# Kernel tuning notes

Hardware: AMD Instinct MI355X
Metric: run time of the kernel (lower is better)

## Reference

```python
import jax, jax.numpy as jnp
import numpy as np

EMB_DIM = 512
NUM_HEADS = 8
HEAD_DIM = EMB_DIM // NUM_HEADS


def setup_inputs() -> dict:
    key = jax.random.key(0)
    ks = jax.random.split(key, 8)
    B, S, D = 2, 192, EMB_DIM
    return {
        "q": jax.random.normal(ks[0], (B, S, D), dtype=jnp.float32),
        "k": jax.random.normal(ks[1], (B, S, D), dtype=jnp.float32),
        "l": jax.random.normal(ks[2], (B, S, D), dtype=jnp.float32),
        "v": jax.random.normal(ks[3], (B, S, D), dtype=jnp.float32),
        "Wq": jax.random.normal(ks[4], (D, D), dtype=jnp.float32) * (1.0 / np.sqrt(D)),
        "Wk": jax.random.normal(ks[5], (D, D), dtype=jnp.float32) * (1.0 / np.sqrt(D)),
        "Wv": jax.random.normal(ks[6], (D, D), dtype=jnp.float32) * (1.0 / np.sqrt(D)),
        "Wout": jax.random.normal(ks[7], (D, D), dtype=jnp.float32) * (1.0 / np.sqrt(D)),
    }


def _heads(x, W):
    # torch nn.Linear: x @ W.T ; then split heads -> (B, H, S, hd)
    B, S, D = x.shape
    y = x @ W.T
    return y.reshape(B, S, NUM_HEADS, HEAD_DIM).transpose(0, 2, 1, 3)


def reference(q, k, l, v, Wq, Wk, Wv, Wout):
    B, QS, D = q.shape
    KS, LS = k.shape[1], l.shape[1]
    qh = _heads(q, Wq)
    kh = _heads(k, Wk)
    lh = _heads(l, Wk)  # NOTE: original module projects l with self.key (faithful)
    vh = _heads(v, Wv)
    # rank-3 attention scores: (B, H, QS, KS, LS)
    scores = jnp.einsum('bhqe,bhke,bhle->bhqkl', qh, kh, lh) / jnp.sqrt(
        jnp.asarray(HEAD_DIM, dtype=q.dtype))
    # softmax jointly over (KS, LS)
    attn = jax.nn.softmax(scores.reshape(B, NUM_HEADS, QS, KS * LS), axis=-1)
    attn = attn.reshape(B, NUM_HEADS, QS, KS, LS)
    # vv[b,h,l,k,d] = v[b,h,k,d]; contract over k and l -> (B, QS, H, hd)
    attended = jnp.einsum('bhqkl,bhkd->bqhd', attn, vh)
    concatenated = attended.reshape(B, QS, EMB_DIM)
    return concatenated @ Wout.T
```

## Files before the change

### kernel.cpp

```cpp
#include <hip/hip_runtime.h>
#include <math.h>

#define BB 2
#define SS 192
#define DD 512
#define HH 8
#define HD 64
#define QCB 6
#define NQC (SS / QCB)
#define PROJ_N (BB*HH*SS*HD)
#define SCL (0.125f * 1.44269504088896f)

typedef __attribute__((ext_vector_type(4))) float f32x4;
typedef _Float16 f16x8 __attribute__((ext_vector_type(8)));

__device__ __forceinline__ f16x8 cvt8_f16_rne(const float* g) {
    f16x8 r;
#pragma unroll
    for (int i = 0; i < 8; ++i) r[i] = (_Float16)g[i];
    return r;
}

__global__ __launch_bounds__(256) void proj4_kernel(
    const float* __restrict__ xq, const float* __restrict__ xk,
    const float* __restrict__ xl, const float* __restrict__ xv,
    const float* __restrict__ Wq, const float* __restrict__ Wk,
    const float* __restrict__ Wv, float* __restrict__ ws,
    float* __restrict__ out) {
    const int p = blockIdx.z;
    const float* x = (p == 0) ? xq : (p == 1) ? xk : (p == 2) ? xl : xv;
    const float* W = (p == 0) ? Wq : (p == 3) ? Wv : Wk;
    float* y = ws + p * PROJ_N;

    __shared__ short Ahs[2][8 * 64 * 8];
    __shared__ short Bhs[2][8 * 64 * 8];

    const int t = threadIdx.x;

    {
        const int bid = (blockIdx.z * gridDim.y + blockIdx.y) * gridDim.x + blockIdx.x;
        for (int i = bid * 256 + t; i < BB * SS * DD; i += 192 * 256) out[i] = 0.f;
    }

    const int lane = t & 63, w = t >> 6;
    const int wr = w >> 1, wc = w & 1;
    const int c16 = lane & 15, q4 = lane >> 4;
    const int m0 = blockIdx.x * 64, n0 = blockIdx.y * 64;
    const int r = t >> 2, cc = t & 3;

    f32x4 acc[2][2];
#pragma unroll
    for (int a = 0; a < 2; ++a)
#pragma unroll
        for (int b = 0; b < 2; ++b) acc[a][b] = (f32x4){0.f, 0.f, 0.f, 0.f};

#define STAGE(kk, bf)                                                               \
    {                                                                               \
        _Pragma("unroll") for (int h2 = 0; h2 < 2; ++h2) {                          \
            const int ec = cc * 2 + h2;                                             \
            float a8[8], w8[8];                                                     \
            *(f32x4*)&a8[0] = *(const f32x4*)&x[(m0 + r) * 512 + (kk) + ec * 8];    \
            *(f32x4*)&a8[4] = *(const f32x4*)&x[(m0 + r) * 512 + (kk) + ec * 8 + 4];\
            *(f32x4*)&w8[0] = *(const f32x4*)&W[(n0 + r) * 512 + (kk) + ec * 8];    \
            *(f32x4*)&w8[4] = *(const f32x4*)&W[(n0 + r) * 512 + (kk) + ec * 8 + 4];\
            *(f16x8*)&Ahs[bf][(ec * 64 + r) * 8] = cvt8_f16_rne(a8);                \
            *(f16x8*)&Bhs[bf][(ec * 64 + r) * 8] = cvt8_f16_rne(w8);                \
        }                                                                           \
    }

    STAGE(0, 0)
    for (int s = 0; s < 8; ++s) {
        __syncthreads();
        if (s + 1 < 8) STAGE((s + 1) * 64, (s + 1) & 1)
        const int b = s & 1;
        f16x8 aH[2][2], bH[2][2];
#pragma unroll
        for (int mt = 0; mt < 2; ++mt) {
            const int row = wr * 32 + mt * 16 + c16;
            aH[mt][0] = *(const f16x8*)&Ahs[b][(q4 * 64 + row) * 8];
            aH[mt][1] = *(const f16x8*)&Ahs[b][((q4 + 4) * 64 + row) * 8];
        }
#pragma unroll
        for (int nt = 0; nt < 2; ++nt) {
            const int col = wc * 32 + nt * 16 + c16;
            bH[nt][0] = *(const f16x8*)&Bhs[b][(q4 * 64 + col) * 8];
            bH[nt][1] = *(const f16x8*)&Bhs[b][((q4 + 4) * 64 + col) * 8];
        }
#pragma unroll
        for (int mt = 0; mt < 2; ++mt)
#pragma unroll
            for (int nt = 0; nt < 2; ++nt) {
                acc[mt][nt] = __builtin_amdgcn_mfma_f32_16x16x32_f16(aH[mt][0], bH[nt][0], acc[mt][nt], 0, 0, 0);
                acc[mt][nt] = __builtin_amdgcn_mfma_f32_16x16x32_f16(aH[mt][1], bH[nt][1], acc[mt][nt], 0, 0, 0);
            }
    }
#undef STAGE

#pragma unroll
    for (int mt = 0; mt < 2; ++mt)
#pragma unroll
        for (int nt = 0; nt < 2; ++nt)
#pragma unroll
            for (int j = 0; j < 4; ++j) {
                const int n_row = m0 + wr * 32 + mt * 16 + q4 * 4 + j;
                const int col = n0 + wc * 32 + nt * 16 + c16;
                const int b = n_row / SS, s2 = n_row % SS;
                const int h = col >> 6, e = col & 63;
                y[((b * HH + h) * SS + s2) * HD + e] = acc[mt][nt][j];
            }
}

__global__ __launch_bounds__(512, 4) void attn3d_mfma_kernel(
    const float* __restrict__ qh, const float* __restrict__ kh,
    const float* __restrict__ lh, const float* __restrict__ vh,
    const float* __restrict__ Wout, float* __restrict__ out) {
    __shared__ short Kf16[8][193][8];
    __shared__ short Lf16[8][193][8];
    __shared__ short qpk[QCB][8][8];
    __shared__ float partial[2][QCB][196];
    __shared__ float Wt[QCB][192];
    __shared__ float attd[16][72];
    __shared__ float zinv[QCB];

    const int blk = blockIdx.x;
    const int bh = blk >> 5, qc = blk & 31;
    const int t = threadIdx.x;
    const int lane = t & 63, w = t >> 6;
    const int lg = w >> 2, kg = w & 3;
    const int c = lane & 15, eh = lane >> 4;

    if (t < QCB * 64) {
        const int q = t >> 6, e = t & 63;
        const float v = qh[(bh * SS + qc * QCB + q) * HD + e] * SCL;
        qpk[q][e >> 3][e & 7] = __builtin_bit_cast(short, (_Float16)v);
    }
#pragma unroll
    for (int j = 0; j < 3; ++j) {
        const int cid = t + 512 * j;
        const int k = cid >> 3, ec = cid & 7;
        float b8[8];
        const float* kp = &kh[(bh * SS + k) * HD + ec * 8];
        *(f32x4*)&b8[0] = *(const f32x4*)&kp[0];
        *(f32x4*)&b8[4] = *(const f32x4*)&kp[4];
        *(f16x8*)&Kf16[ec][k][0] = cvt8_f16_rne(b8);
        const float* lp = &lh[(bh * SS + k) * HD + ec * 8];
        *(f32x4*)&b8[0] = *(const f32x4*)&lp[0];
        *(f32x4*)&b8[4] = *(const f32x4*)&lp[4];
        *(f16x8*)&Lf16[ec][k][0] = cvt8_f16_rne(b8);
    }
    __syncthreads();

    for (int qpi = 0; qpi < 3; ++qpi) {
        const int qa = (qpi + w) % 3;
        const int qb = qa + 3;
        const f16x8 qaf0 = *(const f16x8*)&qpk[qa][eh][0];
        const f16x8 qaf1 = *(const f16x8*)&qpk[qa][4 + eh][0];
        const f16x8 qbf0 = *(const f16x8*)&qpk[qb][eh][0];
        const f16x8 qbf1 = *(const f16x8*)&qpk[qb][4 + eh][0];
        f16x8 Ba[3][2], Bb[3][2];
#pragma unroll
        for (int kt = 0; kt < 3; ++kt) {
            const int col = kg * 48 + kt * 16 + c;
            const f16x8 Kf0 = *(const f16x8*)&Kf16[eh][col][0];
            const f16x8 Kf1 = *(const f16x8*)&Kf16[4 + eh][col][0];
            Ba[kt][0] = Kf0 * qaf0;
            Ba[kt][1] = Kf1 * qaf1;
            Bb[kt][0] = Kf0 * qbf0;
            Bb[kt][1] = Kf1 * qbf1;
        }
        float ra0 = 0.f, ra1 = 0.f, ra2 = 0.f;
        float rb0 = 0.f, rb1 = 0.f, rb2 = 0.f;
#pragma unroll
        for (int lt = 0; lt < 6; ++lt) {
            const int row = lg * 96 + lt * 16 + c;
            const f16x8 A0 = *(const f16x8*)&Lf16[eh][row][0];
            const f16x8 A1 = *(const f16x8*)&Lf16[4 + eh][row][0];
            f32x4 a0 = (f32x4){0.f, 0.f, 0.f, 0.f};
            f32x4 a1 = (f32x4){0.f, 0.f, 0.f, 0.f};
            f32x4 a2 = (f32x4){0.f, 0.f, 0.f, 0.f};
            f32x4 b0 = (f32x4){0.f, 0.f, 0.f, 0.f};
            f32x4 b1 = (f32x4){0.f, 0.f, 0.f, 0.f};
            f32x4 b2 = (f32x4){0.f, 0.f, 0.f, 0.f};
            a0 = __builtin_amdgcn_mfma_f32_16x16x32_f16(A0, Ba[0][0], a0, 0, 0, 0);
            a1 = __builtin_amdgcn_mfma_f32_16x16x32_f16(A0, Ba[1][0], a1, 0, 0, 0);
            a2 = __builtin_amdgcn_mfma_f32_16x16x32_f16(A0, Ba[2][0], a2, 0, 0, 0);
            b0 = __builtin_amdgcn_mfma_f32_16x16x32_f16(A0, Bb[0][0], b0, 0, 0, 0);
            b1 = __builtin_amdgcn_mfma_f32_16x16x32_f16(A0, Bb[1][0], b1, 0, 0, 0);
            b2 = __builtin_amdgcn_mfma_f32_16x16x32_f16(A0, Bb[2][0], b2, 0, 0, 0);
            a0 = __builtin_amdgcn_mfma_f32_16x16x32_f16(A1, Ba[0][1], a0, 0, 0, 0);
            a1 = __builtin_amdgcn_mfma_f32_16x16x32_f16(A1, Ba[1][1], a1, 0, 0, 0);
            a2 = __builtin_amdgcn_mfma_f32_16x16x32_f16(A1, Ba[2][1], a2, 0, 0, 0);
            b0 = __builtin_amdgcn_mfma_f32_16x16x32_f16(A1, Bb[0][1], b0, 0, 0, 0);
            b1 = __builtin_amdgcn_mfma_f32_16x16x32_f16(A1, Bb[1][1], b1, 0, 0, 0);
            b2 = __builtin_amdgcn_mfma_f32_16x16x32_f16(A1, Bb[2][1], b2, 0, 0, 0);
            ra0 += (__builtin_amdgcn_exp2f(a0[0]) + __builtin_amdgcn_exp2f(a0[1])) +
                   (__builtin_amdgcn_exp2f(a0[2]) + __builtin_amdgcn_exp2f(a0[3]));
            ra1 += (__builtin_amdgcn_exp2f(a1[0]) + __builtin_amdgcn_exp2f(a1[1])) +
                   (__builtin_amdgcn_exp2f(a1[2]) + __builtin_amdgcn_exp2f(a1[3]));
            ra2 += (__builtin_amdgcn_exp2f(a2[0]) + __builtin_amdgcn_exp2f(a2[1])) +
                   (__builtin_amdgcn_exp2f(a2[2]) + __builtin_amdgcn_exp2f(a2[3]));
            rb0 += (__builtin_amdgcn_exp2f(b0[0]) + __builtin_amdgcn_exp2f(b0[1])) +
                   (__builtin_amdgcn_exp2f(b0[2]) + __builtin_amdgcn_exp2f(b0[3]));
            rb1 += (__builtin_amdgcn_exp2f(b1[0]) + __builtin_amdgcn_exp2f(b1[1])) +
                   (__builtin_amdgcn_exp2f(b1[2]) + __builtin_amdgcn_exp2f(b1[3]));
            rb2 += (__builtin_amdgcn_exp2f(b2[0]) + __builtin_amdgcn_exp2f(b2[1])) +
                   (__builtin_amdgcn_exp2f(b2[2]) + __builtin_amdgcn_exp2f(b2[3]));
        }
        ra0 += __shfl_xor(ra0, 16, 64);
        ra1 += __shfl_xor(ra1, 16, 64);
        ra2 += __shfl_xor(ra2, 16, 64);
        rb0 += __shfl_xor(rb0, 16, 64);
        rb1 += __shfl_xor(rb1, 16, 64);
        rb2 += __shfl_xor(rb2, 16, 64);
        ra0 += __shfl_xor(ra0, 32, 64);
        ra1 += __shfl_xor(ra1, 32, 64);
        ra2 += __shfl_xor(ra2, 32, 64);
        rb0 += __shfl_xor(rb0, 32, 64);
        rb1 += __shfl_xor(rb1, 32, 64);
        rb2 += __shfl_xor(rb2, 32, 64);
        if (eh == 0) {
            partial[lg][qa][kg * 48 + 0 * 16 + c] = ra0;
            partial[lg][qa][kg * 48 + 1 * 16 + c] = ra1;
            partial[lg][qa][kg * 48 + 2 * 16 + c] = ra2;
            partial[lg][qb][kg * 48 + 0 * 16 + c] = rb0;
            partial[lg][qb][kg * 48 + 1 * 16 + c] = rb1;
            partial[lg][qb][kg * 48 + 2 * 16 + c] = rb2;
        }
    }
    __syncthreads();

    for (int id = t; id < QCB * 192; id += 512) {
        const int q = id / 192, k = id - q * 192;
        Wt[q][k] = partial[0][q][k] + partial[1][q][k];
    }
    for (int id = t; id < 16 * 72; id += 512) ((float*)attd)[id] = 0.f;
    __syncthreads();

    if (w < QCB) {
        const int q = w;
        float z = Wt[q][lane] + Wt[q][lane + 64] + Wt[q][lane + 128];
#pragma unroll
        for (int off = 32; off >= 1; off >>= 1) z += __shfl_xor(z, off, 64);
        if (lane == 0) zinv[q] = 1.f / z;
    }
    __syncthreads();

    if (t < QCB * 64) {
        const int q = t >> 6, d = t & 63;
        const float* vp = vh + bh * SS * HD + d;
        float sum = 0.f;
        for (int k0 = 0; k0 < SS; k0 += 8) {
            float v8[8];
#pragma unroll
            for (int j = 0; j < 8; ++j) v8[j] = vp[(k0 + j) * HD];
#pragma unroll
            for (int j = 0; j < 8; ++j) sum = fmaf(Wt[q][k0 + j], v8[j], sum);
        }
        attd[q][d] = sum * zinv[q];
    }
    __syncthreads();

    const int b = bh >> 3, h = bh & 7;
    f16x8 Ae0, Ae1;
    {
        float a8[8];
        *(f32x4*)&a8[0] = *(const f32x4*)&attd[c][eh * 8];
        *(f32x4*)&a8[4] = *(const f32x4*)&attd[c][eh * 8 + 4];
        Ae0 = cvt8_f16_rne(a8);
        *(f32x4*)&a8[0] = *(const f32x4*)&attd[c][32 + eh * 8];
        *(f32x4*)&a8[4] = *(const f32x4*)&attd[c][32 + eh * 8 + 4];
        Ae1 = cvt8_f16_rne(a8);
    }
#pragma unroll
    for (int jt = 0; jt < 4; ++jt) {
        const int j = (w * 4 + jt) * 16 + c;
        const float* wp = &Wout[j * DD + h * HD];
        float b8[8];
        *(f32x4*)&b8[0] = *(const f32x4*)&wp[eh * 8];
        *(f32x4*)&b8[4] = *(const f32x4*)&wp[eh * 8 + 4];
        const f16x8 B0 = cvt8_f16_rne(b8);
        *(f32x4*)&b8[0] = *(const f32x4*)&wp[32 + eh * 8];
        *(f32x4*)&b8[4] = *(const f32x4*)&wp[32 + eh * 8 + 4];
        const f16x8 B1 = cvt8_f16_rne(b8);
        f32x4 oc = (f32x4){0.f, 0.f, 0.f, 0.f};
        oc = __builtin_amdgcn_mfma_f32_16x16x32_f16(Ae0, B0, oc, 0, 0, 0);
        oc = __builtin_amdgcn_mfma_f32_16x16x32_f16(Ae1, B1, oc, 0, 0, 0);
#pragma unroll
        for (int jj = 0; jj < 4; ++jj) {
            const int q = eh * 4 + jj;
            if (q < QCB)
                atomicAdd(&out[(b * SS + qc * QCB + q) * DD + (w * 4 + jt) * 16 + c], oc[jj]);
        }
    }
}

extern "C" void kernel_launch(void* const* d_in, const int* in_sizes, int n_in,
                              void* d_out, int out_size, void* d_ws, size_t ws_size,
                              hipStream_t stream) {
    (void)in_sizes; (void)n_in; (void)out_size; (void)ws_size;
    const float* q    = (const float*)d_in[0];
    const float* k    = (const float*)d_in[1];
    const float* l    = (const float*)d_in[2];
    const float* v    = (const float*)d_in[3];
    const float* Wq   = (const float*)d_in[4];
    const float* Wk   = (const float*)d_in[5];
    const float* Wv   = (const float*)d_in[6];
    const float* Wout = (const float*)d_in[7];
    float* out = (float*)d_out;

    float* ws  = (float*)d_ws;
    float* qhp = ws + 0 * PROJ_N;
    float* khp = ws + 1 * PROJ_N;
    float* lhp = ws + 2 * PROJ_N;
    float* vhp = ws + 3 * PROJ_N;

    proj4_kernel<<<dim3(384 / 64, 512 / 64, 4), 256, 0, stream>>>(
        q, k, l, v, Wq, Wk, Wv, ws, out);
    attn3d_mfma_kernel<<<dim3(16 * NQC), 512, 0, stream>>>(qhp, khp, lhp, vhp, Wout, out);
}
```

Before: 43.28 us.

## Emit fp16 pre-laid-out Q/K/L from projection to shrink attention load cost

The projection kernel now converts Q (pre-scaled), K and L to fp16 in its epilogue. K and L are written in the padded shared-memory layout the attention kernel uses, so that kernel can copy them straight into LDS with vector loads and no conversion. Each of the 192 attention blocks reloads the full K/L for its head, so this halves the global bytes per block and removes the per-block conversion work. In exchange the projection epilogue does scattered 2-byte stores, which may be less efficient.

```diff
diff --git a/kernel.cpp b/kernel.cpp
--- a/kernel.cpp
+++ b/kernel.cpp
@@ -9,6 +9,7 @@
 #define QCB 6
 #define NQC (SS / QCB)
 #define PROJ_N (BB*HH*SS*HD)
+#define KLPAD (8 * 193 * 8)
 #define SCL (0.125f * 1.44269504088896f)
 
 typedef __attribute__((ext_vector_type(4))) float f32x4;
@@ -19,18 +20,21 @@
 #pragma unroll
     for (int i = 0; i < 8; ++i) r[i] = (_Float16)g[i];
     return r;
+}
+__device__ __forceinline__ short f16s(float v) {
+    return __builtin_bit_cast(short, (_Float16)v);
 }
 
 __global__ __launch_bounds__(256) void proj4_kernel(
     const float* __restrict__ xq, const float* __restrict__ xk,
     const float* __restrict__ xl, const float* __restrict__ xv,
     const float* __restrict__ Wq, const float* __restrict__ Wk,
-    const float* __restrict__ Wv, float* __restrict__ ws,
-    float* __restrict__ out) {
+    const float* __restrict__ Wv, float* __restrict__ vhp,
+    short* __restrict__ qf16, short* __restrict__ khf16,
+    short* __restrict__ lhf16, float* __restrict__ out) {
     const int p = blockIdx.z;
     const float* x = (p == 0) ? xq : (p == 1) ? xk : (p == 2) ? xl : xv;
     const float* W = (p == 0) ? Wq : (p == 3) ? Wv : Wk;
-    float* y = ws + p * PROJ_N;
 
     __shared__ short Ahs[2][8 * 64 * 8];
     __shared__ short Bhs[2][8 * 64 * 8];
@@ -106,13 +110,22 @@
                 const int col = n0 + wc * 32 + nt * 16 + c16;
                 const int b = n_row / SS, s2 = n_row % SS;
                 const int h = col >> 6, e = col & 63;
-                y[((b * HH + h) * SS + s2) * HD + e] = acc[mt][nt][j];
+                const int bh = b * HH + h;
+                const float v = acc[mt][nt][j];
+                if (p == 3) {
+                    vhp[(bh * SS + s2) * HD + e] = v;
+                } else if (p == 0) {
+                    qf16[(bh * SS + s2) * HD + e] = f16s(v * SCL);
+                } else {
+                    short* dst = (p == 1) ? khf16 : lhf16;
+                    dst[bh * KLPAD + (e >> 3) * (193 * 8) + s2 * 8 + (e & 7)] = f16s(v);
+                }
             }
 }
 
 __global__ __launch_bounds__(512, 4) void attn3d_mfma_kernel(
-    const float* __restrict__ qh, const float* __restrict__ kh,
-    const float* __restrict__ lh, const float* __restrict__ vh,
+    const short* __restrict__ qf16, const short* __restrict__ khf16,
+    const short* __restrict__ lhf16, const float* __restrict__ vh,
     const float* __restrict__ Wout, float* __restrict__ out) {
     __shared__ short Kf16[8][193][8];
     __shared__ short Lf16[8][193][8];
@@ -129,24 +142,18 @@
     const int lg = w >> 2, kg = w & 3;
     const int c = lane & 15, eh = lane >> 4;
 
-    if (t < QCB * 64) {
-        const int q = t >> 6, e = t & 63;
-        const float v = qh[(bh * SS + qc * QCB + q) * HD + e] * SCL;
-        qpk[q][e >> 3][e & 7] = __builtin_bit_cast(short, (_Float16)v);
+    if (t < QCB * 8) {
+        const int q = t >> 3, ecj = t & 7;
+        *(f16x8*)&qpk[q][ecj][0] =
+            *(const f16x8*)&qf16[(bh * SS + qc * QCB + q) * HD + ecj * 8];
     }
 #pragma unroll
     for (int j = 0; j < 3; ++j) {
         const int cid = t + 512 * j;
-        const int k = cid >> 3, ec = cid & 7;
-        float b8[8];
-        const float* kp = &kh[(bh * SS + k) * HD + ec * 8];
-        *(f32x4*)&b8[0] = *(const f32x4*)&kp[0];
-        *(f32x4*)&b8[4] = *(const f32x4*)&kp[4];
-        *(f16x8*)&Kf16[ec][k][0] = cvt8_f16_rne(b8);
-        const float* lp = &lh[(bh * SS + k) * HD + ec * 8];
-        *(f32x4*)&b8[0] = *(const f32x4*)&lp[0];
-        *(f32x4*)&b8[4] = *(const f32x4*)&lp[4];
-        *(f16x8*)&Lf16[ec][k][0] = cvt8_f16_rne(b8);
+        const int ec = cid / 192, k2 = cid - ec * 192;
+        const int off = ec * (193 * 8) + k2 * 8;
+        *(f16x8*)&(((short*)Kf16)[off]) = *(const f16x8*)&khf16[bh * KLPAD + off];
+        *(f16x8*)&(((short*)Lf16)[off]) = *(const f16x8*)&lhf16[bh * KLPAD + off];
     }
     __syncthreads();
 
@@ -308,13 +315,14 @@
     const float* Wout = (const float*)d_in[7];
     float* out = (float*)d_out;
 
-    float* ws  = (float*)d_ws;
-    float* qhp = ws + 0 * PROJ_N;
-    float* khp = ws + 1 * PROJ_N;
-    float* lhp = ws + 2 * PROJ_N;
-    float* vhp = ws + 3 * PROJ_N;
+    float* ws    = (float*)d_ws;
+    float* vhp   = ws;
+    short* qf16  = (short*)(ws + PROJ_N);
+    short* khf16 = qf16 + PROJ_N;
+    short* lhf16 = khf16 + 16 * KLPAD;
 
     proj4_kernel<<<dim3(384 / 64, 512 / 64, 4), 256, 0, stream>>>(
-        q, k, l, v, Wq, Wk, Wv, ws, out);
-    attn3d_mfma_kernel<<<dim3(16 * NQC), 512, 0, stream>>>(qhp, khp, lhp, vhp, Wout, out);
-}
+        q, k, l, v, Wq, Wk, Wv, vhp, qf16, khf16, lhf16, out);
+    attn3d_mfma_kernel<<<dim3(16 * NQC), 512, 0, stream>>>(
+        qf16, khf16, lhf16, vhp, Wout, out);
+}
```

New measurement: 42.38 us. 2.1% less time.
